# Kernel tuning notes

Measured on AMD Instinct MI355X. Metric: run time of the kernel, lower is better.

The kernel has to match this reference:

```python
import jax, jax.numpy as jnp
import numpy as np

N_NODES = 50000
N_EDGES = 625000
D = 128


def setup_inputs() -> dict:
    key = jax.random.key(0)
    k1, k2, k3, k4, k5 = jax.random.split(key, 5)
    x = jax.random.normal(k1, (N_NODES, D), dtype=jnp.float32)
    edge_index = jax.random.randint(k2, (2, N_EDGES), 0, N_NODES, dtype=jnp.int32)
    # PyG SAGEConv params: lin_l (applied to aggregated neighbors, with bias),
    # lin_r (root weight, no bias). Stored as [in, out] so we apply x @ W.
    s = 1.0 / np.sqrt(D)
    W_l = jax.random.uniform(k3, (D, D), jnp.float32, -s, s)
    b_l = jax.random.uniform(k4, (D,), jnp.float32, -s, s)
    W_r = jax.random.uniform(k5, (D, D), jnp.float32, -s, s)
    return {"x": x, "edge_index": edge_index, "W_l": W_l, "b_l": b_l, "W_r": W_r}


def sage_conv(x, edge_index, W_l, b_l, W_r):
    src, dst = edge_index[0], edge_index[1]
    # mean aggregation of source features into target nodes
    gathered = x[src]                                            # [E, D]
    summed = jax.ops.segment_sum(gathered, dst, num_segments=N_NODES)   # [N, D]
    deg = jax.ops.segment_sum(jnp.ones((src.shape[0],), jnp.float32), dst,
                              num_segments=N_NODES)              # [N]
    mean = summed / jnp.maximum(deg, 1.0)[:, None]               # [N, D]
    return mean @ W_l + b_l + x @ W_r                            # [N, D]


def reference(x, edge_index, W_l, b_l, W_r):
    # forward: x + relu(SAGEConv(x, edge_index))
    return x + jax.nn.relu(sage_conv(x, edge_index, W_l, b_l, W_r))
```

## Files before the change

### kernel.cpp

```cpp
#include <hip/hip_runtime.h>

#define DF 128
#define GN 16
#define MST 272
#define MAXD 64

typedef __attribute__((ext_vector_type(8))) short short8;
typedef __attribute__((ext_vector_type(4))) float float4v;

__device__ __forceinline__ unsigned int bf16rne(float f) {
    unsigned int u = __float_as_uint(f);
    return (u + 0x7fffu + ((u >> 16) & 1u)) >> 16;
}

__global__ __launch_bounds__(256) void sage_prep(
    const float* __restrict__ x, const int* __restrict__ src,
    const int* __restrict__ dst,
    const float* __restrict__ Wl, const float* __restrict__ Wr,
    int* __restrict__ cnt, int* __restrict__ srt,
    char* __restrict__ xb, char* __restrict__ xq,
    float* __restrict__ rowscale, uint4* __restrict__ Bf,
    int N, int E)
{
    int tid = blockIdx.x * 256 + threadIdx.x;

    if (tid < N * 16) {
        int n = tid >> 4;
        int ln = tid & 15;
        const float4* xp = (const float4*)&x[(size_t)n * DF + ln * 8];
        float4 a = xp[0], b = xp[1];

        uint4 o;
        o.x = bf16rne(a.x) | (bf16rne(a.y) << 16);
        o.y = bf16rne(a.z) | (bf16rne(a.w) << 16);
        o.z = bf16rne(b.x) | (bf16rne(b.y) << 16);
        o.w = bf16rne(b.z) | (bf16rne(b.w) << 16);
        *(uint4*)(xb + (size_t)n * 256 + (size_t)ln * 16) = o;

        float am = fmaxf(fmaxf(fmaxf(fabsf(a.x), fabsf(a.y)),
                               fmaxf(fabsf(a.z), fabsf(a.w))),
                         fmaxf(fmaxf(fabsf(b.x), fabsf(b.y)),
                               fmaxf(fabsf(b.z), fabsf(b.w))));
        #pragma unroll
        for (int s = 1; s < 16; s <<= 1) am = fmaxf(am, __shfl_xor(am, s, 16));
        float scl = am * (1.0f / 127.0f);
        float inv = (am > 0.f) ? 127.0f / am : 0.f;

        int q0 = (int)rintf(a.x * inv), q1 = (int)rintf(a.y * inv);
        int q2 = (int)rintf(a.z * inv), q3 = (int)rintf(a.w * inv);
        int q4 = (int)rintf(b.x * inv), q5 = (int)rintf(b.y * inv);
        int q6 = (int)rintf(b.z * inv), q7 = (int)rintf(b.w * inv);
        uint2 p;
        p.x = (q0 & 255) | ((q1 & 255) << 8) | ((q2 & 255) << 16) | ((unsigned)q3 << 24);
        p.y = (q4 & 255) | ((q5 & 255) << 8) | ((q6 & 255) << 16) | ((unsigned)q7 << 24);
        *(uint2*)(xq + (size_t)n * 128 + (size_t)ln * 8) = p;
        if (ln == 0) rowscale[n] = scl;
    }

    if (tid < E) {
        int d = dst[tid];
        int p = atomicAdd(&cnt[d], 1);
        if (p < MAXD) srt[(size_t)d * MAXD + p] = src[tid];
    }

    if (tid < 4096) {
        int lane = tid & 63;
        int ctks = tid >> 6;
        int ks = ctks >> 3, ct = ctks & 7;
        int q = lane >> 4, m16 = lane & 15;
        int n = ct * 16 + m16;
        unsigned int w[4];
        #pragma unroll
        for (int p2 = 0; p2 < 4; ++p2) {
            int k0 = ks * 32 + q * 8 + p2 * 2;
            float f0 = (k0 < DF) ? Wl[k0 * DF + n] : Wr[(k0 - DF) * DF + n];
            float f1 = (k0 + 1 < DF) ? Wl[(k0 + 1) * DF + n] : Wr[(k0 + 1 - DF) * DF + n];
            w[p2] = bf16rne(f0) | (bf16rne(f1) << 16);
        }
        uint4 o = {w[0], w[1], w[2], w[3]};
        Bf[tid] = o;
    }
}

__device__ __forceinline__ void unp16(uint4 w, float sc, float* a) {
    a[ 0] += sc * (float)((int)(w.x << 24) >> 24);
    a[ 1] += sc * (float)((int)(w.x << 16) >> 24);
    a[ 2] += sc * (float)((int)(w.x <<  8) >> 24);
    a[ 3] += sc * (float)((int)(w.x      ) >> 24);
    a[ 4] += sc * (float)((int)(w.y << 24) >> 24);
    a[ 5] += sc * (float)((int)(w.y << 16) >> 24);
    a[ 6] += sc * (float)((int)(w.y <<  8) >> 24);
    a[ 7] += sc * (float)((int)(w.y      ) >> 24);
    a[ 8] += sc * (float)((int)(w.z << 24) >> 24);
    a[ 9] += sc * (float)((int)(w.z << 16) >> 24);
    a[10] += sc * (float)((int)(w.z <<  8) >> 24);
    a[11] += sc * (float)((int)(w.z      ) >> 24);
    a[12] += sc * (float)((int)(w.w << 24) >> 24);
    a[13] += sc * (float)((int)(w.w << 16) >> 24);
    a[14] += sc * (float)((int)(w.w <<  8) >> 24);
    a[15] += sc * (float)((int)(w.w      ) >> 24);
}

__global__ __launch_bounds__(256) void sage_gg(
    const char* __restrict__ xq, const float* __restrict__ rowscale,
    const char* __restrict__ xb, const int* __restrict__ cnt,
    const int* __restrict__ srt, const uint4* __restrict__ Bf,
    const float* __restrict__ bl,
    float* __restrict__ out, int N)
{
    __shared__ char mlds[GN * MST];
    const int t = threadIdx.x;
    const int nb0 = blockIdx.x * GN;

    {
        const int ln = t & 15;
        const int g  = t >> 4;
        const int h  = ln >> 3;
        const int l8 = ln & 7;
        const int n = nb0 + g;
        const uint4* xq4 = (const uint4*)xq;

        float a[16];
        #pragma unroll
        for (int k = 0; k < 16; ++k) a[k] = 0.f;
        int deg = 1;

        if (n < N) {
            const int start = n * MAXD;
            const int d0 = min(cnt[n], MAXD);
            const int end = start + d0;
            deg = max(d0, 1);

            int sv = 0; float scv = 0.f;
            if (start + ln < end) {
                sv  = srt[start + ln];
                scv = rowscale[sv];
            }

            for (int e0 = start; e0 < end; e0 += 16) {
                int svn = 0; float scvn = 0.f;
                if (e0 + 16 + ln < end) {
                    svn  = srt[e0 + 16 + ln];
                    scvn = rowscale[svn];
                }
                const int m = end - e0;

                uint4 v[8];
                float sc[8];
                #pragma unroll
                for (int j = 0; j < 8; ++j) {
                    int   s = __shfl(sv,  2 * j + h, 16);
                    sc[j]   = __shfl(scv, 2 * j + h, 16);
                    if (2 * j + h < m) {
                        v[j] = xq4[(size_t)s * 8 + l8];
                    }
                }
                #pragma unroll
                for (int j = 0; j < 8; ++j) {
                    if (2 * j + h < m) unp16(v[j], sc[j], a);
                }
                sv = svn; scv = scvn;
            }
        }

        #pragma unroll
        for (int k = 0; k < 16; ++k) a[k] += __shfl_xor(a[k], 8, 16);

        float inv = 1.0f / (float)deg;
        float b0 = h ? a[ 8] : a[ 0];
        float b1 = h ? a[ 9] : a[ 1];
        float b2 = h ? a[10] : a[ 2];
        float b3 = h ? a[11] : a[ 3];
        float b4 = h ? a[12] : a[ 4];
        float b5 = h ? a[13] : a[ 5];
        float b6 = h ? a[14] : a[ 6];
        float b7 = h ? a[15] : a[ 7];
        uint4 o;
        o.x = bf16rne(b0 * inv) | (bf16rne(b1 * inv) << 16);
        o.y = bf16rne(b2 * inv) | (bf16rne(b3 * inv) << 16);
        o.z = bf16rne(b4 * inv) | (bf16rne(b5 * inv) << 16);
        o.w = bf16rne(b6 * inv) | (bf16rne(b7 * inv) << 16);
        *(uint4*)(mlds + g * MST + l8 * 32 + h * 16) = o;
    }
    __syncthreads();

    const int wv = t >> 6;
    const int lane = t & 63;
    const int q = lane >> 4, m16 = lane & 15;
    const int am = min(nb0 + m16, N - 1);
    const short8* arow = (const short8*)(xb + (size_t)am * 256);
    const short8* mrow = (const short8*)(mlds + m16 * MST);
    const short8* bfp  = (const short8*)Bf;

    float4v acc[2];
    #pragma unroll
    for (int c4 = 0; c4 < 2; ++c4) acc[c4] = (float4v){0.f, 0.f, 0.f, 0.f};

    #pragma unroll
    for (int ks = 0; ks < 4; ++ks) {
        short8 af = mrow[ks * 4 + q];
        #pragma unroll
        for (int c4 = 0; c4 < 2; ++c4) {
            int ct = wv * 2 + c4;
            short8 bfrag = bfp[(ks * 8 + ct) * 64 + lane];
            acc[c4] = __builtin_amdgcn_mfma_f32_16x16x32_bf16(af, bfrag, acc[c4], 0, 0, 0);
        }
    }
    #pragma unroll
    for (int ks = 0; ks < 4; ++ks) {
        short8 af = arow[ks * 4 + q];
        #pragma unroll
        for (int c4 = 0; c4 < 2; ++c4) {
            int ct = wv * 2 + c4;
            short8 bfrag = bfp[((ks + 4) * 8 + ct) * 64 + lane];
            acc[c4] = __builtin_amdgcn_mfma_f32_16x16x32_bf16(af, bfrag, acc[c4], 0, 0, 0);
        }
    }

    #pragma unroll
    for (int c4 = 0; c4 < 2; ++c4) {
        int col = (wv * 2 + c4) * 16 + m16;
        float b = bl[col];
        #pragma unroll
        for (int r = 0; r < 4; ++r) {
            int n2 = nb0 + q * 4 + r;
            if (n2 < N) {
                unsigned short xv =
                    *(const unsigned short*)(xb + (size_t)n2 * 256 + col * 2);
                float xf = __uint_as_float((unsigned)xv << 16);
                size_t idx = (size_t)n2 * DF + col;
                out[idx] = xf + fmaxf(acc[c4][r] + b, 0.f);
            }
        }
    }
}

extern "C" void kernel_launch(void* const* d_in, const int* in_sizes, int n_in,
                              void* d_out, int out_size, void* d_ws, size_t ws_size,
                              hipStream_t stream) {
    const float* x  = (const float*)d_in[0];
    const int*   ei = (const int*)d_in[1];
    const float* Wl = (const float*)d_in[2];
    const float* bl = (const float*)d_in[3];
    const float* Wr = (const float*)d_in[4];
    float* out = (float*)d_out;

    const int N = in_sizes[0] / DF;
    const int E = in_sizes[1] / 2;
    const int* src = ei;
    const int* dst = ei + E;

    int* cnt    = (int*)d_ws;
    size_t srtoff = ((size_t)N * 4 + 255) & ~(size_t)255;
    int* srt    = (int*)((char*)d_ws + srtoff);
    size_t bfoff = (srtoff + (size_t)N * MAXD * 4 + 255) & ~(size_t)255;
    uint4* Bf   = (uint4*)((char*)d_ws + bfoff);
    char* xb    = (char*)d_ws + bfoff + 4096 * 16;
    char* xq    = xb + (size_t)N * 256;
    float* rowscale = (float*)(xq + (size_t)N * 128);

    hipMemsetAsync(cnt, 0, (size_t)N * sizeof(int), stream);

    int prepT = N * 16;
    sage_prep<<<(prepT + 255) / 256, 256, 0, stream>>>(
        x, src, dst, Wl, Wr, cnt, srt, xb, xq, rowscale, Bf, N, E);
    sage_gg<<<(N + GN - 1) / GN, 256, 0, stream>>>(
        xq, rowscale, xb, cnt, srt, Bf, bl, out, N);
}
```

Before: 155.2 us.

## Replace global per-edge atomics with two-pass bucketed edge sort via shared histograms

The CSR build no longer does one global atomicAdd per edge into per-node counters. Edges are first binned into groups of 256 destination nodes using per-block shared-memory histograms and one global atomic per group per block. A new kernel then places edges into per-node slots with shared-memory atomics. This cuts global atomic contention and scattered writes but adds a kernel launch and an intermediate buffer. It also packs src into 16 bits and caps each group at 4096 edges, so it assumes N below 65536 and bounded group sizes.

```diff
diff --git a/kernel.cpp b/kernel.cpp
--- a/kernel.cpp
+++ b/kernel.cpp
@@ -4,6 +4,9 @@
 #define GN 16
 #define MST 272
 #define MAXD 64
+#define GSH 8
+#define GCAP 4096
+#define EPB 2048
 
 typedef __attribute__((ext_vector_type(8))) short short8;
 typedef __attribute__((ext_vector_type(4))) float float4v;
@@ -17,50 +20,48 @@
     const float* __restrict__ x, const int* __restrict__ src,
     const int* __restrict__ dst,
     const float* __restrict__ Wl, const float* __restrict__ Wr,
-    int* __restrict__ cnt, int* __restrict__ srt,
+    int* __restrict__ grplen, unsigned int* __restrict__ grpbuf,
     char* __restrict__ xb, char* __restrict__ xq,
     float* __restrict__ rowscale, uint4* __restrict__ Bf,
     int N, int E)
 {
-    int tid = blockIdx.x * 256 + threadIdx.x;
+    __shared__ int hist[256];
+    __shared__ int base[256];
+    const int t = threadIdx.x, b = blockIdx.x;
+    const int tid = b * 256 + t;
+    const int ng = (N + 255) >> GSH;
 
     if (tid < N * 16) {
         int n = tid >> 4;
         int ln = tid & 15;
         const float4* xp = (const float4*)&x[(size_t)n * DF + ln * 8];
-        float4 a = xp[0], b = xp[1];
+        float4 a = xp[0], bb = xp[1];
 
         uint4 o;
         o.x = bf16rne(a.x) | (bf16rne(a.y) << 16);
         o.y = bf16rne(a.z) | (bf16rne(a.w) << 16);
-        o.z = bf16rne(b.x) | (bf16rne(b.y) << 16);
-        o.w = bf16rne(b.z) | (bf16rne(b.w) << 16);
+        o.z = bf16rne(bb.x) | (bf16rne(bb.y) << 16);
+        o.w = bf16rne(bb.z) | (bf16rne(bb.w) << 16);
         *(uint4*)(xb + (size_t)n * 256 + (size_t)ln * 16) = o;
 
         float am = fmaxf(fmaxf(fmaxf(fabsf(a.x), fabsf(a.y)),
                                fmaxf(fabsf(a.z), fabsf(a.w))),
-                         fmaxf(fmaxf(fabsf(b.x), fabsf(b.y)),
-                               fmaxf(fabsf(b.z), fabsf(b.w))));
+                         fmaxf(fmaxf(fabsf(bb.x), fabsf(bb.y)),
+                               fmaxf(fabsf(bb.z), fabsf(bb.w))));
         #pragma unroll
         for (int s = 1; s < 16; s <<= 1) am = fmaxf(am, __shfl_xor(am, s, 16));
         float scl = am * (1.0f / 127.0f);
         float inv = (am > 0.f) ? 127.0f / am : 0.f;
 
-        int q0 = (int)rintf(a.x * inv), q1 = (int)rintf(a.y * inv);
-        int q2 = (int)rintf(a.z * inv), q3 = (int)rintf(a.w * inv);
-        int q4 = (int)rintf(b.x * inv), q5 = (int)rintf(b.y * inv);
-        int q6 = (int)rintf(b.z * inv), q7 = (int)rintf(b.w * inv);
+        int q0 = (int)rintf(a.x * inv),  q1 = (int)rintf(a.y * inv);
+        int q2 = (int)rintf(a.z * inv),  q3 = (int)rintf(a.w * inv);
+        int q4 = (int)rintf(bb.x * inv), q5 = (int)rintf(bb.y * inv);
+        int q6 = (int)rintf(bb.z * inv), q7 = (int)rintf(bb.w * inv);
         uint2 p;
         p.x = (q0 & 255) | ((q1 & 255) << 8) | ((q2 & 255) << 16) | ((unsigned)q3 << 24);
         p.y = (q4 & 255) | ((q5 & 255) << 8) | ((q6 & 255) << 16) | ((unsigned)q7 << 24);
         *(uint2*)(xq + (size_t)n * 128 + (size_t)ln * 8) = p;
         if (ln == 0) rowscale[n] = scl;
-    }
-
-    if (tid < E) {
-        int d = dst[tid];
-        int p = atomicAdd(&cnt[d], 1);
-        if (p < MAXD) srt[(size_t)d * MAXD + p] = src[tid];
     }
 
     if (tid < 4096) {
@@ -80,6 +81,63 @@
         uint4 o = {w[0], w[1], w[2], w[3]};
         Bf[tid] = o;
     }
+
+    const int neb = (E + EPB - 1) / EPB;
+    if (b < neb) {
+        hist[t] = 0;
+        __syncthreads();
+        const int e0 = b * EPB;
+        int d[8], s[8], g[8], r[8];
+        #pragma unroll
+        for (int k = 0; k < 8; ++k) {
+            int e = e0 + k * 256 + t;
+            if (e < E) {
+                d[k] = dst[e];
+                s[k] = src[e];
+                g[k] = d[k] >> GSH;
+                r[k] = atomicAdd(&hist[g[k]], 1);
+            }
+        }
+        __syncthreads();
+        if (t < ng) {
+            int c = hist[t];
+            base[t] = (c > 0) ? atomicAdd(&grplen[t], c) : 0;
+        }
+        __syncthreads();
+        #pragma unroll
+        for (int k = 0; k < 8; ++k) {
+            int e = e0 + k * 256 + t;
+            if (e < E) {
+                int pos = base[g[k]] + r[k];
+                if (pos < GCAP)
+                    grpbuf[(size_t)g[k] * GCAP + pos] =
+                        (unsigned)s[k] | ((unsigned)(d[k] & 255) << 16);
+            }
+        }
+    }
+}
+
+__global__ __launch_bounds__(256) void sage_bucket(
+    const int* __restrict__ grplen, const unsigned int* __restrict__ grpbuf,
+    int* __restrict__ cnt, int* __restrict__ srt, int N)
+{
+    __shared__ int lcnt[256];
+    const int t = threadIdx.x, g = blockIdx.x;
+    lcnt[t] = 0;
+    __syncthreads();
+    const int len = min(grplen[g], GCAP);
+    const unsigned int* seg = grpbuf + (size_t)g * GCAP;
+    for (int i = t; i < len; i += 256) {
+        unsigned int w = seg[i];
+        int s  = (int)(w & 0xFFFFu);
+        int dl = (int)((w >> 16) & 255u);
+        int r = atomicAdd(&lcnt[dl], 1);
+        int node = (g << GSH) + dl;
+        if (r < MAXD) srt[(size_t)node * MAXD + r] = s;
+    }
+    __syncthreads();
+    int node = (g << GSH) + t;
+    if (node < N) cnt[node] = lcnt[t];
 }
 
 __device__ __forceinline__ void unp16(uint4 w, float sc, float* a) {
@@ -249,9 +307,13 @@
     const int E = in_sizes[1] / 2;
     const int* src = ei;
     const int* dst = ei + E;
-
-    int* cnt    = (int*)d_ws;
-    size_t srtoff = ((size_t)N * 4 + 255) & ~(size_t)255;
+    const int ng = (N + 255) >> GSH;
+
+    int* grplen = (int*)d_ws;
+    unsigned int* grpbuf = (unsigned int*)((char*)d_ws + 1024);
+    size_t cntoff = 1024 + (size_t)256 * GCAP * 4;
+    int* cnt    = (int*)((char*)d_ws + cntoff);
+    size_t srtoff = (cntoff + (size_t)N * 4 + 255) & ~(size_t)255;
     int* srt    = (int*)((char*)d_ws + srtoff);
     size_t bfoff = (srtoff + (size_t)N * MAXD * 4 + 255) & ~(size_t)255;
     uint4* Bf   = (uint4*)((char*)d_ws + bfoff);
@@ -259,11 +321,12 @@
     char* xq    = xb + (size_t)N * 256;
     float* rowscale = (float*)(xq + (size_t)N * 128);
 
-    hipMemsetAsync(cnt, 0, (size_t)N * sizeof(int), stream);
+    hipMemsetAsync(grplen, 0, (size_t)ng * sizeof(int), stream);
 
     int prepT = N * 16;
     sage_prep<<<(prepT + 255) / 256, 256, 0, stream>>>(
-        x, src, dst, Wl, Wr, cnt, srt, xb, xq, rowscale, Bf, N, E);
+        x, src, dst, Wl, Wr, grplen, grpbuf, xb, xq, rowscale, Bf, N, E);
+    sage_bucket<<<ng, 256, 0, stream>>>(grplen, grpbuf, cnt, srt, N);
     sage_gg<<<(N + GN - 1) / GN, 256, 0, stream>>>(
         xq, rowscale, xb, cnt, srt, Bf, bl, out, N);
 }
```

Result: faster. 139.5 us (-10.1%).
